# Kernel optimization log

Hardware: AMD Instinct MI355X
Metric: run time of the kernel (lower is better)

The kernel has to match this reference:

```python
import jax, jax.numpy as jnp
import numpy as np

N_HEAD = 8
DROP_RATE = 0.1


def setup_inputs() -> dict:
    key = jax.random.key(0)
    k1, k2, k3 = jax.random.split(key, 3)
    n, c, h, w = 16, 512, 32, 32
    return {
        "x": jax.random.normal(k1, (n, c, h, w), jnp.float32),
        "qkv_w": jax.random.normal(k2, (3 * c, c), jnp.float32) * 0.02,
        "qkv_b": jnp.zeros((3 * c,), jnp.float32),
        "out_w": jax.random.normal(k3, (c, c), jnp.float32) * 0.02,
        "out_b": jnp.zeros((c,), jnp.float32),
        "dropout_enabled": 0,
    }


def reference(x, qkv_w, qkv_b, out_w, out_b, dropout_enabled):
    n, c, h, w = x.shape
    hd = c // N_HEAD  # head dim
    # fused QKV 1x1 conv == per-pixel matmul: [n, 3c, h, w]
    qkv = jnp.einsum('oc,nchw->nohw', qkv_w, x) + qkv_b[None, :, None, None]
    # [n, 3*n_head, hd, h*w] -> [n, 3*n_head, h*w, hd]
    qkv = jnp.swapaxes(qkv.reshape(n, N_HEAD * 3, hd, h * w), 2, 3)
    q, k, v = jnp.split(qkv, 3, axis=1)  # each [n, n_head, hw, hd]
    scale = hd ** (-0.25)
    att = jax.nn.softmax((q * scale) @ (jnp.swapaxes(k, 2, 3) * scale), axis=3)
    y = jnp.swapaxes(att @ v, 2, 3).reshape(n, c, h, w)
    y = jnp.einsum('oc,nchw->nohw', out_w, y) + out_b[None, :, None, None]
    # Dropout2d: drops whole (n, c) channel maps
    rate = DROP_RATE * dropout_enabled
    keep = jax.random.bernoulli(jax.random.key(42), 1.0 - rate, shape=(n, c))
    y = y * keep[..., None, None] / (1.0 - rate)
    return x + y
```

## Files before the change

### kernel.cpp

```cpp
#include <hip/hip_runtime.h>

typedef short bf16x8 __attribute__((ext_vector_type(8)));
typedef float f32x4 __attribute__((ext_vector_type(4)));

#define MFMA16(a,b,c) __builtin_amdgcn_mfma_f32_16x16x32_bf16((a),(b),(c),0,0,0)

static __device__ __forceinline__ unsigned short f2bf(float f){
  unsigned u; __builtin_memcpy(&u, &f, 4);
  u += 0x7fffu + ((u >> 16) & 1u);
  return (unsigned short)(u >> 16);
}
static __device__ __forceinline__ unsigned f32u(float f){
  unsigned u; __builtin_memcpy(&u, &f, 4); return u;
}

static __device__ __forceinline__ void gload_lds16(const void* g, void* l) {
  __builtin_amdgcn_global_load_lds(
      (__attribute__((address_space(1))) void*)g,
      (__attribute__((address_space(3))) void*)l, 16, 0, 0);
}


__global__ __launch_bounds__(256) void cvt_bf16(
    const float* __restrict__ in, unsigned short* __restrict__ out, int n) {
  int i = blockIdx.x * 256 + threadIdx.x;
  if (i < n) out[i] = f2bf(in[i]);
}

__global__ __launch_bounds__(256) void transpose_cvt(
    const float* __restrict__ in, unsigned short* __restrict__ out)
{
  __shared__ unsigned short tile[32][33];
  const long base = (long)blockIdx.z * 512 * 1024;
  const int t = threadIdx.x, tx = t & 31, ty = t >> 5;
  const int c0 = blockIdx.x * 32, r0 = blockIdx.y * 32;
  const float* ib = in + base;
#pragma unroll
  for (int i = 0; i < 4; ++i)
    tile[ty + i * 8][tx] = f2bf(ib[(long)(r0 + ty + i * 8) * 1024 + c0 + tx]);
  __syncthreads();
  unsigned short* ob = out + base;
#pragma unroll
  for (int i = 0; i < 4; ++i)
    ob[(long)(c0 + ty + i * 8) * 512 + r0 + tx] = tile[tx][ty + i * 8];
}

__global__ __launch_bounds__(256, 3) void gemm_qkv(
    const unsigned short* __restrict__ A, const unsigned short* __restrict__ B,
    unsigned short* __restrict__ qkvout, const float* __restrict__ bias)
{
  const int M = 1024, K = 512;
  __shared__ unsigned short As[128 * 64];
  __shared__ unsigned short Bs[128 * 64];
  const int t = threadIdx.x, lane = t & 63, wv = t >> 6;
  const int quad = lane >> 4, ln = lane & 15;
  const int m0 = blockIdx.y * 128, n0 = blockIdx.x * 128;
  const long zb = blockIdx.z;
  A += zb * (long)M * K;

  const int srow = wv * 32 + (lane >> 3);
  const int scol = ((lane & 7) * 8) ^ ((lane >> 3) * 8);

  f32x4 zero = {0.f, 0.f, 0.f, 0.f};
  f32x4 acc[4][4];
#pragma unroll
  for (int i = 0; i < 4; ++i)
#pragma unroll
    for (int j = 0; j < 4; ++j) acc[i][j] = zero;

  const int wm = (wv & 1) * 64, wn = (wv >> 1) * 64;
  const int rsw = (ln & 7) * 8;

  for (int kt = 0; kt < K; kt += 64) {
#pragma unroll
    for (int i = 0; i < 4; ++i) {
      gload_lds16(&A[(long)(m0 + srow + i * 8) * K + kt + scol],
                  &As[(wv * 32 + i * 8) * 64]);
      gload_lds16(&B[(long)(n0 + srow + i * 8) * K + kt + scol],
                  &Bs[(wv * 32 + i * 8) * 64]);
    }
    __syncthreads();
#pragma unroll
    for (int kk = 0; kk < 64; kk += 32) {
      bf16x8 a[4], b[4];
#pragma unroll
      for (int i = 0; i < 4; ++i)
        a[i] = *(const bf16x8*)&As[(wm + i * 16 + ln) * 64 + ((kk + quad * 8) ^ rsw)];
#pragma unroll
      for (int j = 0; j < 4; ++j)
        b[j] = *(const bf16x8*)&Bs[(wn + j * 16 + ln) * 64 + ((kk + quad * 8) ^ rsw)];
#pragma unroll
      for (int i = 0; i < 4; ++i)
#pragma unroll
        for (int j = 0; j < 4; ++j)
          acc[i][j] = MFMA16(a[i], b[j], acc[i][j]);
    }
    __syncthreads();
  }

#pragma unroll
  for (int j = 0; j < 4; ++j) {
    int o = n0 + wn + j * 16 + ln;
    float bb = bias[o];
    int part = o >> 9;
    int h = (o >> 6) & 7, d = o & 63;
    float qs = (part == 0) ? 0.18033688f : 1.0f;
#pragma unroll
    for (int i = 0; i < 4; ++i) {
      int p = m0 + wm + i * 16 + quad * 4;
      f32x4 v = acc[i][j];
      if (part < 2) {
        unsigned short* dst = qkvout + (long)part * 8388608
            + ((long)(zb * 8 + h) * 1024 + p) * 64 + d;
#pragma unroll
        for (int r = 0; r < 4; ++r) dst[r * 64] = f2bf((v[r] + bb) * qs);
      } else {
        long cidx = ((long)zb * 512 + (o - 1024)) * 1024 + p;
        ushort4 st;
        st.x = f2bf(v[0] + bb); st.y = f2bf(v[1] + bb);
        st.z = f2bf(v[2] + bb); st.w = f2bf(v[3] + bb);
        *(ushort4*)&qkvout[16777216 + cidx] = st;
      }
    }
  }
}

__global__ __launch_bounds__(256, 3) void gemm_out(
    const unsigned short* __restrict__ A, const unsigned short* __restrict__ B,
    float* __restrict__ C, const float* __restrict__ bias,
    const float* __restrict__ xin, const int* __restrict__ de_ptr)
{
  const int M = 1024, K = 512;
  __shared__ unsigned short As[128 * 64];
  __shared__ unsigned short Bs[128 * 64];
  const int t = threadIdx.x, lane = t & 63, wv = t >> 6;
  const int quad = lane >> 4, ln = lane & 15;
  const int m0 = blockIdx.y * 128, n0 = blockIdx.x * 128;
  const long zb = blockIdx.z;
  A += zb * (long)M * K;
  C += zb * 512l * M;
  xin += zb * 512l * M;

  const int srow = wv * 32 + (lane >> 3);
  const int scol = ((lane & 7) * 8) ^ ((lane >> 3) * 8);

  f32x4 zero = {0.f, 0.f, 0.f, 0.f};
  f32x4 acc[4][4];
#pragma unroll
  for (int i = 0; i < 4; ++i)
#pragma unroll
    for (int j = 0; j < 4; ++j) acc[i][j] = zero;

  const int wm = (wv & 1) * 64, wn = (wv >> 1) * 64;
  const int rsw = (ln & 7) * 8;

  for (int kt = 0; kt < K; kt += 64) {
#pragma unroll
    for (int i = 0; i < 4; ++i) {
      gload_lds16(&A[(long)(m0 + srow + i * 8) * K + kt + scol],
                  &As[(wv * 32 + i * 8) * 64]);
      gload_lds16(&B[(long)(n0 + srow + i * 8) * K + kt + scol],
                  &Bs[(wv * 32 + i * 8) * 64]);
    }
    __syncthreads();
#pragma unroll
    for (int kk = 0; kk < 64; kk += 32) {
      bf16x8 a[4], b[4];
#pragma unroll
      for (int i = 0; i < 4; ++i)
        a[i] = *(const bf16x8*)&As[(wm + i * 16 + ln) * 64 + ((kk + quad * 8) ^ rsw)];
#pragma unroll
      for (int j = 0; j < 4; ++j)
        b[j] = *(const bf16x8*)&Bs[(wn + j * 16 + ln) * 64 + ((kk + quad * 8) ^ rsw)];
#pragma unroll
      for (int i = 0; i < 4; ++i)
#pragma unroll
        for (int j = 0; j < 4; ++j)
          acc[i][j] = MFMA16(a[i], b[j], acc[i][j]);
    }
    __syncthreads();
  }

  float dscale = 1.0f / (1.0f - 0.1f * (float)de_ptr[0]);

#pragma unroll
  for (int j = 0; j < 4; ++j) {
    int o = n0 + wn + j * 16 + ln;
    float bb = bias[o];
#pragma unroll
    for (int i = 0; i < 4; ++i) {
      int p = m0 + wm + i * 16 + quad * 4;
      long cidx = (long)o * M + p;
      f32x4 v = acc[i][j];
      float4 rx = *(const float4*)&xin[cidx];
      float4 st;
      st.x = rx.x + (v[0] + bb) * dscale;
      st.y = rx.y + (v[1] + bb) * dscale;
      st.z = rx.z + (v[2] + bb) * dscale;
      st.w = rx.w + (v[3] + bb) * dscale;
      *(float4*)&C[cidx] = st;
    }
  }
}

__global__ __launch_bounds__(256, 3) void attn_kernel(
    const unsigned short* __restrict__ q_pd, const unsigned short* __restrict__ k_pd,
    const unsigned short* __restrict__ v_cp, unsigned short* __restrict__ y_pc)
{
  __shared__ unsigned short Ks[128 * 64];
  __shared__ unsigned short Vs[64 * 128];
  __shared__ unsigned short Ps[4 * 16 * 136];
  const int t = threadIdx.x, lane = t & 63, wv = t >> 6;
  const int quad = lane >> 4, ln = lane & 15;
  const int nh = blockIdx.y, n = nh >> 3, h = nh & 7;
  const int q0 = blockIdx.x * 128;

  bf16x8 qa[2][2];
#pragma unroll
  for (int s2 = 0; s2 < 2; ++s2) {
    const unsigned short* qb =
        q_pd + ((long)nh * 1024 + q0 + s2 * 64 + wv * 16 + ln) * 64;
    qa[s2][0] = *(const bf16x8*)(qb + quad * 8);
    qa[s2][1] = *(const bf16x8*)(qb + 32 + quad * 8);
  }

  f32x4 zero = {0.f, 0.f, 0.f, 0.f};
  float l_acc[2] = {0.f, 0.f};
  f32x4 o_acc[2][4];
#pragma unroll
  for (int s2 = 0; s2 < 2; ++s2)
#pragma unroll
    for (int nf = 0; nf < 4; ++nf) o_acc[s2][nf] = zero;

  const unsigned short* kg0 = k_pd + (long)nh * 1024 * 64;
  const unsigned short* vg0 = v_cp + ((long)n * 512 + h * 64) * 1024;
  unsigned short* Pw = &Ps[wv * 16 * 136];

  const int krow = lane >> 3;
  const int kcol = ((lane & 7) * 8) ^ ((lane >> 3) * 8);
  const int vrow = lane >> 4;
  const int rsw = (ln & 7) * 8;

  for (int c = 0; c < 8; ++c) {
    const unsigned short* kg = kg0 + (long)c * 128 * 64;
    const unsigned short* vg = vg0 + c * 128;
#pragma unroll
    for (int i = 0; i < 4; ++i) {
      const int vcol = ((lane & 15) * 8) ^ ((((i * 4) + vrow) & 7) * 8);
      gload_lds16(kg + (long)(wv * 32 + i * 8 + krow) * 64 + kcol,
                  &Ks[(wv * 32 + i * 8) * 64]);
      gload_lds16(vg + (long)(wv * 16 + i * 4 + vrow) * 1024 + vcol,
                  &Vs[(wv * 16 + i * 4) * 128]);
    }
    __syncthreads();

    bf16x8 ap[2][4];
#pragma unroll
    for (int s2 = 0; s2 < 2; ++s2) {
      f32x4 s[8];
#pragma unroll
      for (int j = 0; j < 8; ++j) {
        bf16x8 ka0 = *(const bf16x8*)&Ks[(j * 16 + ln) * 64 + ((quad * 8) ^ rsw)];
        bf16x8 ka1 = *(const bf16x8*)&Ks[(j * 16 + ln) * 64 + ((32 + quad * 8) ^ rsw)];
        f32x4 sj = MFMA16(ka0, qa[s2][0], zero);
        s[j] = MFMA16(ka1, qa[s2][1], sj);
      }
      float ls = 0.f;
#pragma unroll
      for (int j = 0; j < 8; ++j)
#pragma unroll
        for (int r = 0; r < 4; ++r) {
          float pv = __builtin_amdgcn_exp2f(s[j][r]);
          s[j][r] = pv;
          ls += pv;
        }
      l_acc[s2] += ls;
#pragma unroll
      for (int j = 0; j < 8; ++j) {
        uint2 pk;
        pk.x = __builtin_amdgcn_perm(f32u(s[j][1]), f32u(s[j][0]), 0x07060302u);
        pk.y = __builtin_amdgcn_perm(f32u(s[j][3]), f32u(s[j][2]), 0x07060302u);
        *(uint2*)&Pw[ln * 136 + j * 16 + quad * 4] = pk;
      }
#pragma unroll
      for (int k2 = 0; k2 < 4; ++k2)
        ap[s2][k2] = *(const bf16x8*)&Pw[ln * 136 + k2 * 32 + quad * 8];
    }

#pragma unroll
    for (int nf = 0; nf < 4; ++nf)
#pragma unroll
      for (int k2 = 0; k2 < 4; ++k2) {
        bf16x8 va = *(const bf16x8*)&Vs[(nf * 16 + ln) * 128 + ((k2 * 32 + quad * 8) ^ rsw)];
        o_acc[0][nf] = MFMA16(va, ap[0][k2], o_acc[0][nf]);
        o_acc[1][nf] = MFMA16(va, ap[1][k2], o_acc[1][nf]);
      }
    __syncthreads();
  }

#pragma unroll
  for (int s2 = 0; s2 < 2; ++s2) {
    float la = l_acc[s2];
    la += __shfl_xor(la, 16);
    la += __shfl_xor(la, 32);
    float linv = 1.0f / la;
    const int p = q0 + s2 * 64 + wv * 16 + ln;
    unsigned short* yb = y_pc + ((long)n * 1024 + p) * 512 + h * 64 + quad * 4;
#pragma unroll
    for (int nf = 0; nf < 4; ++nf) {
      ushort4 st;
      st.x = f2bf(o_acc[s2][nf][0] * linv);
      st.y = f2bf(o_acc[s2][nf][1] * linv);
      st.z = f2bf(o_acc[s2][nf][2] * linv);
      st.w = f2bf(o_acc[s2][nf][3] * linv);
      *(ushort4*)&yb[nf * 16] = st;
    }
  }
}

extern "C" void kernel_launch(void* const* d_in, const int* in_sizes, int n_in,
                              void* d_out, int out_size, void* d_ws, size_t ws_size,
                              hipStream_t stream) {
  (void)in_sizes; (void)n_in; (void)out_size; (void)ws_size;
  const float* x     = (const float*)d_in[0];
  const float* qkv_w = (const float*)d_in[1];
  const float* qkv_b = (const float*)d_in[2];
  const float* out_w = (const float*)d_in[3];
  const float* out_b = (const float*)d_in[4];
  const int* de = (const int*)d_in[5];
  float* out = (float*)d_out;
  unsigned short* ws = (unsigned short*)d_ws;

  unsigned short* xT   = ws;
  unsigned short* qkv  = ws + 8388608;
  unsigned short* y_pc = ws;
  unsigned short* wq   = ws + 33554432;
  unsigned short* wo   = wq + 786432;

  cvt_bf16<<<3072, 256, 0, stream>>>(qkv_w, wq, 786432);
  cvt_bf16<<<1024, 256, 0, stream>>>(out_w, wo, 262144);

  transpose_cvt<<<dim3(32, 16, 16), 256, 0, stream>>>(x, xT);

  gemm_qkv<<<dim3(12, 8, 16), 256, 0, stream>>>(xT, wq, qkv, qkv_b);

  attn_kernel<<<dim3(8, 128), 256, 0, stream>>>(
      qkv, qkv + 8388608, qkv + 16777216, y_pc);

  gemm_out<<<dim3(4, 8, 16), 256, 0, stream>>>(
      y_pc, wo, out, out_b, x, de);
}
```

Baseline: 212.3 us.

## Rewrite attention with 32x32 MFMA, register P repack, and double-buffered K/V

The attention kernel moves from 16x16x32 to 32x32x16 bf16 MFMA tiles. Each block now covers 256 queries, and each wave handles 64 queries in two 32-row groups. The softmax probabilities are packed to bf16 with v_cvt_pk_bf16_f32 and rearranged with v_permlane32_swap in registers, so the P round trip through LDS is gone. K/V tiles are double-buffered so the next chunk's global-to-LDS load overlaps compute, and the grid is reordered to group heads. The cost is more LDS and registers per block, with occupancy lowered to 2 blocks per CU.

```diff
diff --git a/kernel.cpp b/kernel.cpp
--- a/kernel.cpp
+++ b/kernel.cpp
@@ -2,16 +2,24 @@
 
 typedef short bf16x8 __attribute__((ext_vector_type(8)));
 typedef float f32x4 __attribute__((ext_vector_type(4)));
+typedef float f32x16 __attribute__((ext_vector_type(16)));
 
 #define MFMA16(a,b,c) __builtin_amdgcn_mfma_f32_16x16x32_bf16((a),(b),(c),0,0,0)
+#define MFMA32(a,b,c) __builtin_amdgcn_mfma_f32_32x32x16_bf16((a),(b),(c),0,0,0)
 
 static __device__ __forceinline__ unsigned short f2bf(float f){
   unsigned u; __builtin_memcpy(&u, &f, 4);
   u += 0x7fffu + ((u >> 16) & 1u);
   return (unsigned short)(u >> 16);
 }
-static __device__ __forceinline__ unsigned f32u(float f){
-  unsigned u; __builtin_memcpy(&u, &f, 4); return u;
+
+static __device__ __forceinline__ unsigned cvtpk(float lo, float hi){
+  unsigned r;
+  asm volatile("v_cvt_pk_bf16_f32 %0, %1, %2" : "=v"(r) : "v"(lo), "v"(hi));
+  return r;
+}
+static __device__ __forceinline__ void pl32swap(unsigned &a, unsigned &b){
+  asm volatile("v_permlane32_swap_b32 %0, %1" : "+v"(a), "+v"(b));
 }
 
 static __device__ __forceinline__ void gload_lds16(const void* g, void* l) {
@@ -19,7 +27,6 @@
       (__attribute__((address_space(1))) void*)g,
       (__attribute__((address_space(3))) void*)l, 16, 0, 0);
 }
-
 
 __global__ __launch_bounds__(256) void cvt_bf16(
     const float* __restrict__ in, unsigned short* __restrict__ out, int n) {
@@ -203,117 +210,143 @@
   }
 }
 
-__global__ __launch_bounds__(256, 3) void attn_kernel(
+__global__ __launch_bounds__(256, 2) void attn_kernel(
     const unsigned short* __restrict__ q_pd, const unsigned short* __restrict__ k_pd,
     const unsigned short* __restrict__ v_cp, unsigned short* __restrict__ y_pc)
 {
-  __shared__ unsigned short Ks[128 * 64];
-  __shared__ unsigned short Vs[64 * 128];
-  __shared__ unsigned short Ps[4 * 16 * 136];
+  __shared__ unsigned short Ks[2][128 * 64];
+  __shared__ unsigned short Vs[2][64 * 128];
   const int t = threadIdx.x, lane = t & 63, wv = t >> 6;
-  const int quad = lane >> 4, ln = lane & 15;
-  const int nh = blockIdx.y, n = nh >> 3, h = nh & 7;
-  const int q0 = blockIdx.x * 128;
-
-  bf16x8 qa[2][2];
-#pragma unroll
-  for (int s2 = 0; s2 < 2; ++s2) {
+  const int l31 = lane & 31, bh8 = (lane >> 5) * 8;
+  const int qt = blockIdx.y >> 5;
+  const int nh = blockIdx.x * 32 + (blockIdx.y & 31);
+  const int n = nh >> 3, h = nh & 7;
+  const int q0 = qt * 256;
+
+  bf16x8 qa[2][4];
+#pragma unroll
+  for (int qg = 0; qg < 2; ++qg) {
     const unsigned short* qb =
-        q_pd + ((long)nh * 1024 + q0 + s2 * 64 + wv * 16 + ln) * 64;
-    qa[s2][0] = *(const bf16x8*)(qb + quad * 8);
-    qa[s2][1] = *(const bf16x8*)(qb + 32 + quad * 8);
-  }
-
-  f32x4 zero = {0.f, 0.f, 0.f, 0.f};
+        q_pd + ((long)nh * 1024 + q0 + wv * 64 + qg * 32 + l31) * 64;
+#pragma unroll
+    for (int ds = 0; ds < 4; ++ds)
+      qa[qg][ds] = *(const bf16x8*)(qb + ds * 16 + bh8);
+  }
+
+  f32x16 zacc;
+#pragma unroll
+  for (int r = 0; r < 16; ++r) zacc[r] = 0.f;
+  f32x16 o_acc[2][2];
+  o_acc[0][0] = zacc; o_acc[0][1] = zacc; o_acc[1][0] = zacc; o_acc[1][1] = zacc;
   float l_acc[2] = {0.f, 0.f};
-  f32x4 o_acc[2][4];
-#pragma unroll
-  for (int s2 = 0; s2 < 2; ++s2)
-#pragma unroll
-    for (int nf = 0; nf < 4; ++nf) o_acc[s2][nf] = zero;
 
   const unsigned short* kg0 = k_pd + (long)nh * 1024 * 64;
   const unsigned short* vg0 = v_cp + ((long)n * 512 + h * 64) * 1024;
-  unsigned short* Pw = &Ps[wv * 16 * 136];
 
   const int krow = lane >> 3;
   const int kcol = ((lane & 7) * 8) ^ ((lane >> 3) * 8);
   const int vrow = lane >> 4;
-  const int rsw = (ln & 7) * 8;
+  const int rsw = (lane & 7) * 8;
+
+#pragma unroll
+  for (int i = 0; i < 4; ++i) {
+    const int vcol = ((lane & 15) * 8) ^ ((((i * 4) + vrow) & 7) * 8);
+    gload_lds16(kg0 + (long)(wv * 32 + i * 8 + krow) * 64 + kcol,
+                &Ks[0][(wv * 32 + i * 8) * 64]);
+    gload_lds16(vg0 + (long)(wv * 16 + i * 4 + vrow) * 1024 + vcol,
+                &Vs[0][(wv * 16 + i * 4) * 128]);
+  }
+  __syncthreads();
+
+  union U { bf16x8 v; unsigned u[4]; };
+  auto sm_pack = [&](const f32x16& sv, bf16x8* paq, float& lac) {
+    float e[16];
+#pragma unroll
+    for (int r = 0; r < 16; ++r) e[r] = __builtin_amdgcn_exp2f(sv[r]);
+    float ls = 0.f;
+#pragma unroll
+    for (int r = 0; r < 16; ++r) ls += e[r];
+    lac += ls;
+    unsigned pk4[4][2];
+#pragma unroll
+    for (int hh = 0; hh < 4; ++hh) {
+      pk4[hh][0] = cvtpk(e[4 * hh + 0], e[4 * hh + 1]);
+      pk4[hh][1] = cvtpk(e[4 * hh + 2], e[4 * hh + 3]);
+    }
+#pragma unroll
+    for (int hk = 0; hk < 2; ++hk) {
+      unsigned a0 = pk4[2 * hk + 1][0], b0 = pk4[2 * hk][0];
+      unsigned a1 = pk4[2 * hk + 1][1], b1 = pk4[2 * hk][1];
+      pl32swap(a0, b0); pl32swap(a1, b1);
+      U u; u.u[0] = b0; u.u[1] = b1; u.u[2] = a0; u.u[3] = a1;
+      paq[hk] = u.v;
+    }
+  };
 
   for (int c = 0; c < 8; ++c) {
-    const unsigned short* kg = kg0 + (long)c * 128 * 64;
-    const unsigned short* vg = vg0 + c * 128;
-#pragma unroll
-    for (int i = 0; i < 4; ++i) {
-      const int vcol = ((lane & 15) * 8) ^ ((((i * 4) + vrow) & 7) * 8);
-      gload_lds16(kg + (long)(wv * 32 + i * 8 + krow) * 64 + kcol,
-                  &Ks[(wv * 32 + i * 8) * 64]);
-      gload_lds16(vg + (long)(wv * 16 + i * 4 + vrow) * 1024 + vcol,
-                  &Vs[(wv * 16 + i * 4) * 128]);
-    }
-    __syncthreads();
-
-    bf16x8 ap[2][4];
-#pragma unroll
-    for (int s2 = 0; s2 < 2; ++s2) {
-      f32x4 s[8];
-#pragma unroll
-      for (int j = 0; j < 8; ++j) {
-        bf16x8 ka0 = *(const bf16x8*)&Ks[(j * 16 + ln) * 64 + ((quad * 8) ^ rsw)];
-        bf16x8 ka1 = *(const bf16x8*)&Ks[(j * 16 + ln) * 64 + ((32 + quad * 8) ^ rsw)];
-        f32x4 sj = MFMA16(ka0, qa[s2][0], zero);
-        s[j] = MFMA16(ka1, qa[s2][1], sj);
+    const int cur = c & 1;
+    if (c < 7) {
+      const unsigned short* kg = kg0 + (long)(c + 1) * 128 * 64;
+      const unsigned short* vg = vg0 + (c + 1) * 128;
+      unsigned short* KsD = Ks[cur ^ 1];
+      unsigned short* VsD = Vs[cur ^ 1];
+#pragma unroll
+      for (int i = 0; i < 4; ++i) {
+        const int vcol = ((lane & 15) * 8) ^ ((((i * 4) + vrow) & 7) * 8);
+        gload_lds16(kg + (long)(wv * 32 + i * 8 + krow) * 64 + kcol,
+                    &KsD[(wv * 32 + i * 8) * 64]);
+        gload_lds16(vg + (long)(wv * 16 + i * 4 + vrow) * 1024 + vcol,
+                    &VsD[(wv * 16 + i * 4) * 128]);
       }
-      float ls = 0.f;
-#pragma unroll
-      for (int j = 0; j < 8; ++j)
-#pragma unroll
-        for (int r = 0; r < 4; ++r) {
-          float pv = __builtin_amdgcn_exp2f(s[j][r]);
-          s[j][r] = pv;
-          ls += pv;
+    }
+    const unsigned short* KsC = Ks[cur];
+    const unsigned short* VsC = Vs[cur];
+
+#pragma unroll
+    for (int kgi = 0; kgi < 4; ++kgi) {
+      f32x16 s0 = zacc, s1 = zacc;
+#pragma unroll
+      for (int ds = 0; ds < 4; ++ds) {
+        bf16x8 ka = *(const bf16x8*)&KsC[(kgi * 32 + l31) * 64 + ((ds * 16 + bh8) ^ rsw)];
+        s0 = MFMA32(ka, qa[0][ds], s0);
+        s1 = MFMA32(ka, qa[1][ds], s1);
+      }
+      bf16x8 pa[2][2];
+      sm_pack(s0, pa[0], l_acc[0]);
+      sm_pack(s1, pa[1], l_acc[1]);
+#pragma unroll
+      for (int dg = 0; dg < 2; ++dg)
+#pragma unroll
+        for (int hk = 0; hk < 2; ++hk) {
+          bf16x8 va = *(const bf16x8*)
+              &VsC[(dg * 32 + l31) * 128 + (((kgi * 2 + hk) * 16 + bh8) ^ rsw)];
+          o_acc[dg][0] = MFMA32(va, pa[0][hk], o_acc[dg][0]);
+          o_acc[dg][1] = MFMA32(va, pa[1][hk], o_acc[dg][1]);
         }
-      l_acc[s2] += ls;
-#pragma unroll
-      for (int j = 0; j < 8; ++j) {
-        uint2 pk;
-        pk.x = __builtin_amdgcn_perm(f32u(s[j][1]), f32u(s[j][0]), 0x07060302u);
-        pk.y = __builtin_amdgcn_perm(f32u(s[j][3]), f32u(s[j][2]), 0x07060302u);
-        *(uint2*)&Pw[ln * 136 + j * 16 + quad * 4] = pk;
-      }
-#pragma unroll
-      for (int k2 = 0; k2 < 4; ++k2)
-        ap[s2][k2] = *(const bf16x8*)&Pw[ln * 136 + k2 * 32 + quad * 8];
-    }
-
-#pragma unroll
-    for (int nf = 0; nf < 4; ++nf)
-#pragma unroll
-      for (int k2 = 0; k2 < 4; ++k2) {
-        bf16x8 va = *(const bf16x8*)&Vs[(nf * 16 + ln) * 128 + ((k2 * 32 + quad * 8) ^ rsw)];
-        o_acc[0][nf] = MFMA16(va, ap[0][k2], o_acc[0][nf]);
-        o_acc[1][nf] = MFMA16(va, ap[1][k2], o_acc[1][nf]);
-      }
-    __syncthreads();
-  }
-
-#pragma unroll
-  for (int s2 = 0; s2 < 2; ++s2) {
-    float la = l_acc[s2];
-    la += __shfl_xor(la, 16);
+    }
+    __syncthreads();
+  }
+
+#pragma unroll
+  for (int qg = 0; qg < 2; ++qg) {
+    float la = l_acc[qg];
     la += __shfl_xor(la, 32);
     float linv = 1.0f / la;
-    const int p = q0 + s2 * 64 + wv * 16 + ln;
-    unsigned short* yb = y_pc + ((long)n * 1024 + p) * 512 + h * 64 + quad * 4;
-#pragma unroll
-    for (int nf = 0; nf < 4; ++nf) {
-      ushort4 st;
-      st.x = f2bf(o_acc[s2][nf][0] * linv);
-      st.y = f2bf(o_acc[s2][nf][1] * linv);
-      st.z = f2bf(o_acc[s2][nf][2] * linv);
-      st.w = f2bf(o_acc[s2][nf][3] * linv);
-      *(ushort4*)&yb[nf * 16] = st;
+    const int q = q0 + wv * 64 + qg * 32 + l31;
+    unsigned short* yb = y_pc + ((long)n * 1024 + q) * 512 + h * 64;
+#pragma unroll
+    for (int dg = 0; dg < 2; ++dg) {
+      f32x16 o = o_acc[dg][qg];
+#pragma unroll
+      for (int rq = 0; rq < 4; ++rq) {
+        int d0 = dg * 32 + rq * 8 + (bh8 >> 1);
+        ushort4 st;
+        st.x = f2bf(o[rq * 4 + 0] * linv);
+        st.y = f2bf(o[rq * 4 + 1] * linv);
+        st.z = f2bf(o[rq * 4 + 2] * linv);
+        st.w = f2bf(o[rq * 4 + 3] * linv);
+        *(ushort4*)&yb[d0] = st;
+      }
     }
   }
 }
@@ -344,7 +377,7 @@
 
   gemm_qkv<<<dim3(12, 8, 16), 256, 0, stream>>>(xT, wq, qkv, qkv_b);
 
-  attn_kernel<<<dim3(8, 128), 256, 0, stream>>>(
+  attn_kernel<<<dim3(4, 128), 256, 0, stream>>>(
       qkv, qkv + 8388608, qkv + 16777216, y_pc);
 
   gemm_out<<<dim3(4, 8, 16), 256, 0, stream>>>(
```

Result: faster. 206.9 us (-2.5%).
